# Performance work log

Hardware: AMD Instinct MI355X
Metric: run time of the kernel (lower is better)

The kernel has to match this reference:

```python
import jax, jax.numpy as jnp
import numpy as np

N_NODES = 50000
N_EDGES = 1600000
D_IN, H, Z = 2000, 128, 32
BN_EPS = 1e-5


def setup_inputs() -> dict:
    key = jax.random.key(0)
    ks = jax.random.split(key, 10)
    x = jax.random.normal(ks[0], (N_NODES, D_IN), dtype=jnp.float32)
    edge_index = jax.random.randint(ks[1], (2, N_EDGES), 0, N_NODES, dtype=jnp.int32)
    def xavier(k, shape):
        fan_in, fan_out = shape
        s = jnp.sqrt(6.0 / (fan_in + fan_out))
        return jax.random.uniform(k, shape, jnp.float32, -s, s)
    return {
        "x": x,
        "edge_index": edge_index,
        "W1": xavier(ks[2], (D_IN, H)), "b1": jnp.zeros((H,), jnp.float32),
        "W2": xavier(ks[3], (H, H)),   "b2": jnp.zeros((H,), jnp.float32),
        "g1": jnp.ones((H,), jnp.float32), "be1": jnp.zeros((H,), jnp.float32),
        "g2": jnp.ones((H,), jnp.float32), "be2": jnp.zeros((H,), jnp.float32),
        "Wm": xavier(ks[4], (H, Z)), "bm": jnp.zeros((Z,), jnp.float32),
        "Wv": xavier(ks[5], (H, Z)), "bv": jnp.zeros((Z,), jnp.float32),
        "Wt": xavier(ks[6], (H, 1)), "bt": jnp.zeros((1,), jnp.float32),
        "eps": jax.random.normal(ks[7], (N_NODES, Z), dtype=jnp.float32),
    }


def _gcn_norm(edge_index, n):
    # add self-loops, compute symmetric normalization D^-1/2 A D^-1/2
    loop = jnp.arange(n, dtype=edge_index.dtype)
    src = jnp.concatenate([edge_index[0], loop])
    dst = jnp.concatenate([edge_index[1], loop])
    deg = jax.ops.segment_sum(jnp.ones_like(src, dtype=jnp.float32), dst, num_segments=n)
    dinv = jnp.where(deg > 0, jax.lax.rsqrt(deg), 0.0)
    norm = dinv[src] * dinv[dst]  # [E+N]
    return src, dst, norm


def _gcn(h, W, b, src, dst, norm, n):
    h = h @ W                               # [N, out]
    msg = h[src] * norm[:, None]            # gather + scale, [E+N, out]
    out = jax.ops.segment_sum(msg, dst, num_segments=n)  # scatter-add
    return out + b


def _bn(h, g, b):
    # batch-norm over node dim (training statistics, biased var like torch)
    mu = jnp.mean(h, axis=0)
    var = jnp.mean((h - mu) ** 2, axis=0)
    return g * (h - mu) * jax.lax.rsqrt(var + BN_EPS) + b


def reference(x, edge_index, W1, b1, W2, b2, g1, be1, g2, be2, Wm, bm, Wv, bv, Wt, bt, eps):
    n = x.shape[0]
    src, dst, norm = _gcn_norm(edge_index, n)
    # layer 0: GCN -> BN -> ReLU (dropout = identity in eval)
    h = jax.nn.relu(_bn(_gcn(x, W1, b1, src, dst, norm, n), g1, be1))
    residual = h
    # layer 1
    h = jax.nn.relu(_bn(_gcn(h, W2, b2, src, dst, norm, n), g2, be2))
    h = h + residual
    t = jax.nn.sigmoid(h @ Wt + bt)                       # [N, 1]
    q_m = _gcn(h, Wm, bm, src, dst, norm, n)              # [N, Z]
    q_s = _gcn(h, Wv, bv, src, dst, norm, n)              # [N, Z]
    std = jax.nn.softplus(q_s) + 1e-6
    q_z = q_m + std * eps                                 # Normal(q_m, std).rsample()
    return q_z, q_m, q_s, t
```

## Files before the change

kernel.cpp:

```cpp
#include <hip/hip_runtime.h>
#include <hip/hip_bf16.h>
#include <math.h>

#define N_NODES 50000
#define N_EDGES 1600000
#define DIN     2000
#define HDIM    128
#define ZDIM    32
#define AGG_GRID 782
#define PADROW  50000
#define MAXDEG  96

#define OFF_HA     0UL
#define OFF_HB     12804096UL
#define OFF_H0RES  25608192UL
#define OFF_HMV    38412288UL
#define OFF_W1T    44814336UL
#define OFF_W2T    45338624UL
#define OFF_W3T    45371392UL
#define OFF_CSR    45387776UL
#define OFF_CNT    64587776UL
#define OFF_SUMSA  64787776UL
#define OFF_SUMSB  64788800UL

typedef __attribute__((ext_vector_type(8))) short short8;
typedef __attribute__((ext_vector_type(4))) float f32x4;

__device__ inline unsigned short f2bf(float f) {
    unsigned u = __builtin_bit_cast(unsigned, f);
    u += 0x7FFFu + ((u >> 16) & 1u);
    return (unsigned short)(u >> 16);
}
__device__ inline float bf2f(unsigned short u) {
    return __builtin_bit_cast(float, ((unsigned)u) << 16);
}
__device__ inline void ubf2(unsigned u, float& lo, float& hi) {
    lo = __builtin_bit_cast(float, u << 16);
    hi = __builtin_bit_cast(float, u & 0xFFFF0000u);
}
__device__ inline void unpack8(uint4 v, float* f) {
    ubf2(v.x, f[0], f[1]); ubf2(v.y, f[2], f[3]);
    ubf2(v.z, f[4], f[5]); ubf2(v.w, f[6], f[7]);
}
__device__ inline void gload_lds16(const unsigned short* g, unsigned short* l) {
    __builtin_amdgcn_global_load_lds(
        (const __attribute__((address_space(1))) unsigned int*)g,
        (__attribute__((address_space(3))) unsigned int*)l, 16, 0, 0);
}
__device__ inline f32x4 mfma16(short8 a, short8 b, f32x4 c) {
    return __builtin_amdgcn_mfma_f32_16x16x32_bf16(a, b, c, 0, 0, 0);
}

__global__ void k_prep(const int* __restrict__ e_src, const int* __restrict__ e_dst,
                       const float* __restrict__ W1, const float* __restrict__ W2,
                       const float* __restrict__ Wm, const float* __restrict__ Wv,
                       unsigned short* __restrict__ W1t, unsigned short* __restrict__ W2t,
                       unsigned short* __restrict__ W3t,
                       int* __restrict__ cnt, int* __restrict__ csr,
                       unsigned short* __restrict__ HA, unsigned short* __restrict__ HMV) {
    const int b = blockIdx.x;
    const int tid = threadIdx.x;
    for (int g = b * 256 + tid; g < N_EDGES / 4; g += 1121 * 256) {
        int4 s4 = *(const int4*)(e_src + (size_t)g * 4);
        int4 d4 = *(const int4*)(e_dst + (size_t)g * 4);
        const int ss[4] = {s4.x, s4.y, s4.z, s4.w};
        const int dd[4] = {d4.x, d4.y, d4.z, d4.w};
#pragma unroll
        for (int q = 0; q < 4; ++q) {
            int p = atomicAdd(&cnt[dd[q]], 1);
            if (p < MAXDEG) csr[dd[q] * MAXDEG + p] = ss[q];
        }
    }
    if (b < 1024) {
        int idx = b * 256 + tid;
        int n = idx >> 11, k = idx & 2047;
        W1t[idx] = f2bf((k < DIN) ? W1[(size_t)k * HDIM + n] : 0.f);
    } else if (b < 1088) {
        int idx = (b - 1024) * 256 + tid;
        int n = idx >> 7, k = idx & 127;
        W2t[idx] = f2bf(W2[(size_t)k * HDIM + n]);
    } else if (b < 1120) {
        int idx = (b - 1088) * 256 + tid;
        int n = idx >> 7, k = idx & 127;
        W3t[idx] = f2bf((n < 32) ? Wm[(size_t)k * ZDIM + n]
                                 : Wv[(size_t)k * ZDIM + (n - 32)]);
    } else if (b == 1120) {
        uint4 z = make_uint4(0, 0, 0, 0);
        if (tid < 256)
            *(uint4*)(HA + (size_t)PADROW * HDIM + tid * 8) = z;
        if (tid < 128)
            *(uint4*)(HMV + (size_t)PADROW * 64 + tid * 8) = z;
    }
}

#define G1_BM 64
#define G1_BK 64
__global__ __launch_bounds__(256) void k_gemm1m(const float* __restrict__ A,
        const unsigned short* __restrict__ Bt, const int* __restrict__ cnt,
        unsigned short* __restrict__ C) {
    __shared__ __align__(16) unsigned short Abuf[2][G1_BM * G1_BK];
    __shared__ __align__(16) unsigned short Bbuf[2][HDIM * G1_BK];
    const int tid  = threadIdx.x;
    const int lane = tid & 63;
    const int wave = tid >> 6;
    const int m0   = blockIdx.x * G1_BM;
    const int wm   = (wave >> 1) * 32;
    const int wn   = (wave & 1) * 64;
    const int ar   = tid >> 2;
    const int acp  = tid & 3;

    f32x4 acc[2][4];
#pragma unroll
    for (int i = 0; i < 2; ++i)
#pragma unroll
        for (int j = 0; j < 4; ++j) acc[i][j] = (f32x4)0.f;

    float areg[16];

    auto stageA = [&](int k0) {
        const int g = m0 + ar;
        const int kk = k0 + acp * 16;
        if (g < N_NODES && kk < DIN) {
#pragma unroll
            for (int q = 0; q < 4; ++q)
                *(float4*)&areg[q * 4] = *(const float4*)(A + (size_t)g * DIN + kk + q * 4);
        } else {
#pragma unroll
            for (int q = 0; q < 16; ++q) areg[q] = 0.f;
        }
    };

    auto writeA = [&](int c) {
        unsigned short u[16];
#pragma unroll
        for (int q = 0; q < 16; ++q) u[q] = f2bf(areg[q]);
#pragma unroll
        for (int q = 0; q < 2; ++q) {
            int chunk = acp * 2 + q;
            int pos = chunk ^ (ar & 7);
            *(uint4*)&Abuf[c][ar * G1_BK + pos * 8] = *(const uint4*)&u[q * 8];
        }
    };

    auto issueB = [&](int k0, int c) {
#pragma unroll
        for (int q = 0; q < 4; ++q) {
            int nbase = wave * 32 + q * 8;
            int n = nbase + (lane >> 3);
            int pos = lane & 7;
            int ksrc = k0 + ((pos ^ (n & 7)) * 8);
            gload_lds16(Bt + (size_t)n * 2048 + ksrc, &Bbuf[c][nbase * G1_BK]);
        }
    };

    auto compute = [&](int c) {
        const int rl = lane & 15;
        const int kg = lane >> 4;
#pragma unroll
        for (int ks = 0; ks < 2; ++ks) {
            short8 a[2], b[4];
#pragma unroll
            for (int i = 0; i < 2; ++i) {
                int r = wm + i * 16 + rl;
                int pos = (kg + ks * 4) ^ (r & 7);
                a[i] = *(const short8*)&Abuf[c][r * G1_BK + pos * 8];
            }
#pragma unroll
            for (int j = 0; j < 4; ++j) {
                int n = wn + j * 16 + rl;
                int pos = (kg + ks * 4) ^ (n & 7);
                b[j] = *(const short8*)&Bbuf[c][n * G1_BK + pos * 8];
            }
#pragma unroll
            for (int i = 0; i < 2; ++i)
#pragma unroll
                for (int j = 0; j < 4; ++j)
                    acc[i][j] = mfma16(a[i], b[j], acc[i][j]);
        }
    };

    const int NT = 32;
    stageA(0);
    issueB(0, 0);
#pragma unroll 1
    for (int t = 0; t < NT; ++t) {
        const int c = t & 1;
        writeA(c);
        __syncthreads();
        if (t + 1 < NT) { stageA((t + 1) * G1_BK); issueB((t + 1) * G1_BK, c ^ 1); }
        compute(c);
        __syncthreads();
    }
#pragma unroll
    for (int i = 0; i < 2; ++i) {
        int rb = m0 + wm + i * 16 + (lane >> 4) * 4;
        float dv[4];
#pragma unroll
        for (int r = 0; r < 4; ++r)
            dv[r] = (rb + r < N_NODES) ? rsqrtf((float)(cnt[rb + r] + 1)) : 0.f;
#pragma unroll
        for (int j = 0; j < 4; ++j) {
            int col = wn + j * 16 + (lane & 15);
#pragma unroll
            for (int r = 0; r < 4; ++r)
                if (rb + r < N_NODES)
                    C[(size_t)(rb + r) * HDIM + col] = f2bf(dv[r] * acc[i][j][r]);
        }
    }
}

__global__ __launch_bounds__(256) void k_aggs(const unsigned short* __restrict__ h,
        const int* __restrict__ cnt, const int* __restrict__ csr,
        unsigned short* __restrict__ out, float* __restrict__ sums) {
    __shared__ float redS[8][128];
    __shared__ float redQ[8][128];
    const int tid = threadIdx.x;
    const int slot = tid >> 5;
    const int l32 = tid & 31;
    const int team = l32 >> 4;
    const int lg = l32 & 15;
    const int c = lg * 8;
    float ssum[8] = {}, sq[8] = {};
#pragma unroll 1
    for (int base = blockIdx.x * 8; base < N_NODES; base += AGG_GRID * 8) {
        const int row = base + slot;
        if (row >= N_NODES) continue;
        const int deg = cnt[row];
        const float di = rsqrtf((float)(deg + 1));
        float a[8] = {};
        if (team == 0) {
            float hv[8];
            unpack8(*(const uint4*)(h + (size_t)row * HDIM + c), hv);
#pragma unroll
            for (int i = 0; i < 8; ++i) a[i] = hv[i];
        }
        const int nch = (deg + 3) >> 2;
        const int half = (nch + 1) >> 1;
        const int jb = team ? half : 0;
        const int je = team ? nch : half;
        const int4* csr4 = (const int4*)csr + (size_t)row * (MAXDEG / 4);
        int4 cur = make_int4(PADROW, PADROW, PADROW, PADROW), nxt = cur;
        if (jb < je) cur = csr4[jb];
#pragma unroll 1
        for (int j = jb; j < je; ++j) {
            if (j + 1 < je) nxt = csr4[j + 1];
            const int e0 = 4 * j;
            int s0 = cur.x;
            int s1 = (e0 + 1 < deg) ? cur.y : PADROW;
            int s2 = (e0 + 2 < deg) ? cur.z : PADROW;
            int s3 = (e0 + 3 < deg) ? cur.w : PADROW;
            uint4 g0 = *(const uint4*)(h + (size_t)s0 * HDIM + c);
            uint4 g1 = *(const uint4*)(h + (size_t)s1 * HDIM + c);
            uint4 g2 = *(const uint4*)(h + (size_t)s2 * HDIM + c);
            uint4 g3 = *(const uint4*)(h + (size_t)s3 * HDIM + c);
            float v[8];
            unpack8(g0, v);
#pragma unroll
            for (int i = 0; i < 8; ++i) a[i] += v[i];
            unpack8(g1, v);
#pragma unroll
            for (int i = 0; i < 8; ++i) a[i] += v[i];
            unpack8(g2, v);
#pragma unroll
            for (int i = 0; i < 8; ++i) a[i] += v[i];
            unpack8(g3, v);
#pragma unroll
            for (int i = 0; i < 8; ++i) a[i] += v[i];
            cur = nxt;
        }
#pragma unroll
        for (int i = 0; i < 8; ++i) a[i] += __shfl_xor(a[i], 16);
        if (team == 0) {
            unsigned short o[8];
#pragma unroll
            for (int i = 0; i < 8; ++i) {
                float ov = di * a[i];
                o[i] = f2bf(ov);
                ssum[i] += ov;
                sq[i] += ov * ov;
            }
            *(uint4*)(out + (size_t)row * HDIM + c) = *(const uint4*)o;
        }
    }
    if (team == 0) {
#pragma unroll
        for (int i = 0; i < 8; i += 4) {
            *(float4*)&redS[slot][c + i] = *(const float4*)&ssum[i];
            *(float4*)&redQ[slot][c + i] = *(const float4*)&sq[i];
        }
    }
    __syncthreads();
    if (tid < 128) {
        float s = 0.f, q = 0.f;
#pragma unroll
        for (int g = 0; g < 8; ++g) { s += redS[g][tid]; q += redQ[g][tid]; }
        atomicAdd(&sums[tid], s);
        atomicAdd(&sums[128 + tid], q);
    }
}

__global__ __launch_bounds__(256) void k_gemm2m(const unsigned short* __restrict__ Ain,
        const unsigned short* __restrict__ W2t, const float* __restrict__ sums,
        const float* __restrict__ gg, const float* __restrict__ beta,
        const int* __restrict__ cnt,
        unsigned short* __restrict__ h0res, unsigned short* __restrict__ Hout) {
    __shared__ __align__(16) unsigned short As[64 * 128];
    __shared__ __align__(16) unsigned short Bs[128 * 128];
    __shared__ float prm[256];
    const int tid = threadIdx.x, lane = tid & 63, wave = tid >> 6;
    const int m0 = blockIdx.x * 64;
    if (tid < 128) {
        float mean = sums[tid] * (1.f / N_NODES);
        float var = sums[128 + tid] * (1.f / N_NODES) - mean * mean;
        float rstd = rsqrtf(var + 1e-5f);
        float sc = gg[tid] * rstd;
        prm[tid] = sc;
        prm[128 + tid] = beta[tid] - mean * sc;
    }
    __syncthreads();
    {
        const int ar = tid >> 2, acp = tid & 3;
        const int g = m0 + ar;
        unsigned short u[32];
        if (g < N_NODES) {
#pragma unroll
            for (int q = 0; q < 4; ++q) {
                int kb = acp * 32 + q * 8;
                float v[8];
                unpack8(*(const uint4*)(Ain + (size_t)g * HDIM + kb), v);
#pragma unroll
                for (int e = 0; e < 8; ++e)
                    u[q * 8 + e] = f2bf(fmaxf(v[e] * prm[kb + e] + prm[128 + kb + e], 0.f));
            }
#pragma unroll
            for (int q = 0; q < 4; ++q)
                *(uint4*)(h0res + (size_t)g * HDIM + acp * 32 + q * 8) = *(const uint4*)&u[q * 8];
        } else {
#pragma unroll
            for (int q = 0; q < 32; ++q) u[q] = 0;
        }
#pragma unroll
        for (int q = 0; q < 4; ++q) {
            int ch = acp * 4 + q;
            int pos = ch ^ (ar & 7);
            *(uint4*)&As[ar * 128 + pos * 8] = *(const uint4*)&u[q * 8];
        }
    }
    {
        const int br = tid >> 1, half = tid & 1;
#pragma unroll
        for (int q = 0; q < 8; ++q) {
            int ch = half * 8 + q;
            int pos = ch ^ (br & 7);
            *(uint4*)&Bs[br * 128 + pos * 8] =
                *(const uint4*)(W2t + (size_t)br * 128 + ch * 8);
        }
    }
    __syncthreads();
    const int wm = (wave >> 1) * 32, wn = (wave & 1) * 64;
    const int rl = lane & 15, kg = lane >> 4;
    f32x4 acc[2][4];
#pragma unroll
    for (int i = 0; i < 2; ++i)
#pragma unroll
        for (int j = 0; j < 4; ++j) acc[i][j] = (f32x4)0.f;
#pragma unroll
    for (int ks = 0; ks < 4; ++ks) {
        short8 a[2], b[4];
        int ch = ks * 4 + kg;
#pragma unroll
        for (int i = 0; i < 2; ++i) {
            int r = wm + i * 16 + rl;
            a[i] = *(const short8*)&As[r * 128 + (ch ^ (r & 7)) * 8];
        }
#pragma unroll
        for (int j = 0; j < 4; ++j) {
            int n = wn + j * 16 + rl;
            b[j] = *(const short8*)&Bs[n * 128 + (ch ^ (n & 7)) * 8];
        }
#pragma unroll
        for (int i = 0; i < 2; ++i)
#pragma unroll
            for (int j = 0; j < 4; ++j) acc[i][j] = mfma16(a[i], b[j], acc[i][j]);
    }
#pragma unroll
    for (int i = 0; i < 2; ++i) {
        int rb = m0 + wm + i * 16 + (lane >> 4) * 4;
        float dv[4];
#pragma unroll
        for (int r = 0; r < 4; ++r)
            dv[r] = (rb + r < N_NODES) ? rsqrtf((float)(cnt[rb + r] + 1)) : 0.f;
#pragma unroll
        for (int j = 0; j < 4; ++j) {
            int col = wn + j * 16 + rl;
#pragma unroll
            for (int r = 0; r < 4; ++r)
                if (rb + r < N_NODES)
                    Hout[(size_t)(rb + r) * HDIM + col] = f2bf(dv[r] * acc[i][j][r]);
        }
    }
}

__global__ __launch_bounds__(256) void k_gemm3m(const unsigned short* __restrict__ Ain,
        const unsigned short* __restrict__ h0res, const float* __restrict__ sums,
        const float* __restrict__ gg, const float* __restrict__ beta,
        const unsigned short* __restrict__ W3t, const float* __restrict__ Wt,
        const float* __restrict__ bt, const int* __restrict__ cnt,
        unsigned short* __restrict__ hmv, float* __restrict__ t_out) {
    __shared__ __align__(16) unsigned short As[64 * 128];
    __shared__ __align__(16) unsigned short Bs[64 * 128];
    __shared__ float WtS[128];
    __shared__ float prm[256];
    const int tid = threadIdx.x, lane = tid & 63, wave = tid >> 6;
    const int m0 = blockIdx.x * 64;
    if (tid < 128) {
        float mean = sums[tid] * (1.f / N_NODES);
        float var = sums[128 + tid] * (1.f / N_NODES) - mean * mean;
        float rstd = rsqrtf(var + 1e-5f);
        float sc = gg[tid] * rstd;
        prm[tid] = sc;
        prm[128 + tid] = beta[tid] - mean * sc;
        WtS[tid] = Wt[tid];
    }
    __syncthreads();
    {
        const int ar = tid >> 2, acp = tid & 3;
        const int g = m0 + ar;
        unsigned short u[32];
        if (g < N_NODES) {
#pragma unroll
            for (int q = 0; q < 4; ++q) {
                int kb = acp * 32 + q * 8;
                float v[8], rr[8];
                unpack8(*(const uint4*)(Ain + (size_t)g * HDIM + kb), v);
                unpack8(*(const uint4*)(h0res + (size_t)g * HDIM + kb), rr);
#pragma unroll
                for (int e = 0; e < 8; ++e)
                    u[q * 8 + e] =
                        f2bf(fmaxf(v[e] * prm[kb + e] + prm[128 + kb + e], 0.f) + rr[e]);
            }
        } else {
#pragma unroll
            for (int q = 0; q < 32; ++q) u[q] = 0;
        }
#pragma unroll
        for (int q = 0; q < 4; ++q) {
            int ch = acp * 4 + q;
            int pos = ch ^ (ar & 7);
            *(uint4*)&As[ar * 128 + pos * 8] = *(const uint4*)&u[q * 8];
        }
    }
    {
        const int br = tid >> 2, chq = tid & 3;
#pragma unroll
        for (int q = 0; q < 4; ++q) {
            int ch = chq * 4 + q;
            int pos = ch ^ (br & 7);
            *(uint4*)&Bs[br * 128 + pos * 8] =
                *(const uint4*)(W3t + (size_t)br * 128 + ch * 8);
        }
    }
    __syncthreads();
    const int wm = (wave >> 1) * 32, wn = (wave & 1) * 32;
    const int rl = lane & 15, kg = lane >> 4;
    f32x4 acc[2][2];
#pragma unroll
    for (int i = 0; i < 2; ++i)
#pragma unroll
        for (int j = 0; j < 2; ++j) acc[i][j] = (f32x4)0.f;
#pragma unroll
    for (int ks = 0; ks < 4; ++ks) {
        short8 a[2], b[2];
        int ch = ks * 4 + kg;
#pragma unroll
        for (int i = 0; i < 2; ++i) {
            int r = wm + i * 16 + rl;
            a[i] = *(const short8*)&As[r * 128 + (ch ^ (r & 7)) * 8];
        }
#pragma unroll
        for (int j = 0; j < 2; ++j) {
            int n = wn + j * 16 + rl;
            b[j] = *(const short8*)&Bs[n * 128 + (ch ^ (n & 7)) * 8];
        }
#pragma unroll
        for (int i = 0; i < 2; ++i)
#pragma unroll
            for (int j = 0; j < 2; ++j) acc[i][j] = mfma16(a[i], b[j], acc[i][j]);
    }
#pragma unroll
    for (int i = 0; i < 2; ++i) {
        int rb = m0 + wm + i * 16 + (lane >> 4) * 4;
        float dv[4];
#pragma unroll
        for (int r = 0; r < 4; ++r)
            dv[r] = (rb + r < N_NODES) ? rsqrtf((float)(cnt[rb + r] + 1)) : 0.f;
#pragma unroll
        for (int j = 0; j < 2; ++j) {
            int col = wn + j * 16 + rl;
#pragma unroll
            for (int r = 0; r < 4; ++r)
                if (rb + r < N_NODES)
                    hmv[(size_t)(rb + r) * 64 + col] = f2bf(dv[r] * acc[i][j][r]);
        }
    }
    {
        const int r = wave * 16 + (lane & 15);
        const int sub = lane >> 4;
        float s = 0.f;
#pragma unroll
        for (int q = 0; q < 4; ++q) {
            int ch = sub * 4 + q;
            short8 v = *(const short8*)&As[r * 128 + (ch ^ (r & 7)) * 8];
#pragma unroll
            for (int e = 0; e < 8; ++e)
                s += bf2f((unsigned short)v[e]) * WtS[ch * 8 + e];
        }
        s += __shfl_xor(s, 16);
        s += __shfl_xor(s, 32);
        if (sub == 0 && (m0 + r) < N_NODES)
            t_out[m0 + r] = 1.f / (1.f + expf(-(s + bt[0])));
    }
}

__global__ __launch_bounds__(256) void k_aggfin(const unsigned short* __restrict__ hmv,
        const int* __restrict__ cnt, const int* __restrict__ csr,
        const float* __restrict__ bm, const float* __restrict__ bv,
        const float* __restrict__ eps,
        float* __restrict__ out_qz, float* __restrict__ out_qm,
        float* __restrict__ out_qs) {
    const int tid = threadIdx.x;
    const int slot = tid >> 4;
    const int l16 = tid & 15;
    const int team = l16 >> 3;
    const int l = l16 & 7;
    const int c = l * 8;
#pragma unroll 1
    for (int base = blockIdx.x * 16; base < N_NODES; base += AGG_GRID * 16) {
        const int row = base + slot;
        if (row >= N_NODES) continue;
        const int deg = cnt[row];
        const float di = rsqrtf((float)(deg + 1));
        float a[8] = {};
        if (team == 0) {
            float hv[8];
            unpack8(*(const uint4*)(hmv + (size_t)row * 64 + c), hv);
#pragma unroll
            for (int i = 0; i < 8; ++i) a[i] = hv[i];
        }
        const int nch = (deg + 3) >> 2;
        const int half = (nch + 1) >> 1;
        const int jb = team ? half : 0;
        const int je = team ? nch : half;
        const int4* csr4 = (const int4*)csr + (size_t)row * (MAXDEG / 4);
        int4 cur = make_int4(PADROW, PADROW, PADROW, PADROW), nxt = cur;
        if (jb < je) cur = csr4[jb];
#pragma unroll 1
        for (int j = jb; j < je; ++j) {
            if (j + 1 < je) nxt = csr4[j + 1];
            const int e0 = 4 * j;
            int s0 = cur.x;
            int s1 = (e0 + 1 < deg) ? cur.y : PADROW;
            int s2 = (e0 + 2 < deg) ? cur.z : PADROW;
            int s3 = (e0 + 3 < deg) ? cur.w : PADROW;
            uint4 g0 = *(const uint4*)(hmv + (size_t)s0 * 64 + c);
            uint4 g1 = *(const uint4*)(hmv + (size_t)s1 * 64 + c);
            uint4 g2 = *(const uint4*)(hmv + (size_t)s2 * 64 + c);
            uint4 g3 = *(const uint4*)(hmv + (size_t)s3 * 64 + c);
            float v[8];
            unpack8(g0, v);
#pragma unroll
            for (int i = 0; i < 8; ++i) a[i] += v[i];
            unpack8(g1, v);
#pragma unroll
            for (int i = 0; i < 8; ++i) a[i] += v[i];
            unpack8(g2, v);
#pragma unroll
            for (int i = 0; i < 8; ++i) a[i] += v[i];
            unpack8(g3, v);
#pragma unroll
            for (int i = 0; i < 8; ++i) a[i] += v[i];
            cur = nxt;
        }
#pragma unroll
        for (int i = 0; i < 8; ++i) a[i] += __shfl_xor(a[i], 8);
        const bool lo = l < 4;
        float qv[8];
#pragma unroll
        for (int i = 0; i < 8; ++i)
            qv[i] = di * a[i] + (lo ? bm[c + i] : bv[c - 32 + i]);
        float sp[8] = {};
        if (!lo) {
#pragma unroll
            for (int i = 0; i < 8; ++i)
                sp[i] = fmaxf(qv[i], 0.f) + log1pf(expf(-fabsf(qv[i]))) + 1e-6f;
        }
        float spx[8];
#pragma unroll
        for (int i = 0; i < 8; ++i) spx[i] = __shfl_xor(sp[i], 4);
        if (team == 0) {
            if (lo) {
                *(float4*)(out_qm + (size_t)row * 32 + c) = *(const float4*)&qv[0];
                *(float4*)(out_qm + (size_t)row * 32 + c + 4) = *(const float4*)&qv[4];
                float e[8];
                *(float4*)&e[0] = *(const float4*)(eps + (size_t)row * 32 + c);
                *(float4*)&e[4] = *(const float4*)(eps + (size_t)row * 32 + c + 4);
                float qz[8];
#pragma unroll
                for (int i = 0; i < 8; ++i) qz[i] = qv[i] + spx[i] * e[i];
                *(float4*)(out_qz + (size_t)row * 32 + c) = *(const float4*)&qz[0];
                *(float4*)(out_qz + (size_t)row * 32 + c + 4) = *(const float4*)&qz[4];
            } else {
                *(float4*)(out_qs + (size_t)row * 32 + (c - 32)) = *(const float4*)&qv[0];
                *(float4*)(out_qs + (size_t)row * 32 + (c - 32) + 4) = *(const float4*)&qv[4];
            }
        }
    }
}

extern "C" void kernel_launch(void* const* d_in, const int* in_sizes, int n_in,
                              void* d_out, int out_size, void* d_ws, size_t ws_size,
                              hipStream_t stream) {
    (void)in_sizes; (void)n_in; (void)out_size; (void)ws_size;
    const float* x   = (const float*)d_in[0];
    const int*   ei  = (const int*)d_in[1];
    const float* W1  = (const float*)d_in[2];
    const float* W2  = (const float*)d_in[4];
    const float* g1  = (const float*)d_in[6];
    const float* be1 = (const float*)d_in[7];
    const float* g2  = (const float*)d_in[8];
    const float* be2 = (const float*)d_in[9];
    const float* Wm  = (const float*)d_in[10];
    const float* bm  = (const float*)d_in[11];
    const float* Wv  = (const float*)d_in[12];
    const float* bv  = (const float*)d_in[13];
    const float* Wt  = (const float*)d_in[14];
    const float* bt  = (const float*)d_in[15];
    const float* eps = (const float*)d_in[16];

    const int* e_src = ei;
    const int* e_dst = ei + N_EDGES;

    char* ws = (char*)d_ws;
    unsigned short* HA    = (unsigned short*)(ws + OFF_HA);
    unsigned short* HB    = (unsigned short*)(ws + OFF_HB);
    unsigned short* H0RES = (unsigned short*)(ws + OFF_H0RES);
    unsigned short* HMV   = (unsigned short*)(ws + OFF_HMV);
    unsigned short* W1t   = (unsigned short*)(ws + OFF_W1T);
    unsigned short* W2t   = (unsigned short*)(ws + OFF_W2T);
    unsigned short* W3t   = (unsigned short*)(ws + OFF_W3T);
    int*   csr     = (int*)(ws + OFF_CSR);
    int*   cnt     = (int*)(ws + OFF_CNT);
    float* sumsA   = (float*)(ws + OFF_SUMSA);
    float* sumsB   = (float*)(ws + OFF_SUMSB);

    float* out_qz = (float*)d_out;
    float* out_qm = out_qz + N_NODES * ZDIM;
    float* out_qs = out_qm + N_NODES * ZDIM;
    float* out_t  = out_qs + N_NODES * ZDIM;

    const int MB = (N_NODES + 63) / 64;

    hipMemsetAsync(ws + OFF_CNT, 0, 200000, stream);
    hipMemsetAsync(ws + OFF_SUMSA, 0, 2048, stream);
    k_prep<<<1121, 256, 0, stream>>>(e_src, e_dst, W1, W2, Wm, Wv,
                                     W1t, W2t, W3t, cnt, csr, HA, HMV);
    k_gemm1m<<<MB, 256, 0, stream>>>(x, W1t, cnt, HA);
    k_aggs<<<AGG_GRID, 256, 0, stream>>>(HA, cnt, csr, HB, sumsA);
    k_gemm2m<<<MB, 256, 0, stream>>>(HB, W2t, sumsA, g1, be1, cnt, H0RES, HA);
    k_aggs<<<AGG_GRID, 256, 0, stream>>>(HA, cnt, csr, HB, sumsB);
    k_gemm3m<<<MB, 256, 0, stream>>>(HB, H0RES, sumsB, g2, be2, W3t, Wt, bt,
                                     cnt, HMV, out_t);
    k_aggfin<<<AGG_GRID, 256, 0, stream>>>(HMV, cnt, csr, bm, bv, eps,
                                           out_qz, out_qm, out_qs);
}
```

Measured before the change: 463.7 us.

## Partition aggregation columns by XCD and deepen GEMM1 A-prefetch to two tiles

The aggregation kernel now gives each block a 32-column quarter of the feature dimension. Block indices are mapped so that each group of XCDs (block id mod 8) always handles the same column quarter, which shrinks the per-XCD L2 working set for the gathered neighbor rows. It also regroups threads so that 8 threads cover one row, 32 rows per block, and reduces the BN statistics per quarter. Separately, GEMM1 keeps two register buffers for A and prefetches two k-tiles ahead to hide global load latency, at the cost of more registers and extra loop unrolling.

Result: slower. 475.5 us (+2.6%).

```diff
diff --git a/kernel.cpp b/kernel.cpp
--- a/kernel.cpp
+++ b/kernel.cpp
@@ -8,6 +8,7 @@
 #define HDIM    128
 #define ZDIM    32
 #define AGG_GRID 782
+#define AGQ_GRID 1024
 #define PADROW  50000
 #define MAXDEG  96
 
@@ -115,25 +116,25 @@
 #pragma unroll
         for (int j = 0; j < 4; ++j) acc[i][j] = (f32x4)0.f;
 
-    float areg[16];
-
-    auto stageA = [&](int k0) {
+    float areg0[16], areg1[16];
+
+    auto stageA = [&](int k0, float* a) {
         const int g = m0 + ar;
         const int kk = k0 + acp * 16;
         if (g < N_NODES && kk < DIN) {
 #pragma unroll
             for (int q = 0; q < 4; ++q)
-                *(float4*)&areg[q * 4] = *(const float4*)(A + (size_t)g * DIN + kk + q * 4);
+                *(float4*)&a[q * 4] = *(const float4*)(A + (size_t)g * DIN + kk + q * 4);
         } else {
 #pragma unroll
-            for (int q = 0; q < 16; ++q) areg[q] = 0.f;
+            for (int q = 0; q < 16; ++q) a[q] = 0.f;
         }
     };
 
-    auto writeA = [&](int c) {
+    auto writeA = [&](int c, const float* a) {
         unsigned short u[16];
 #pragma unroll
-        for (int q = 0; q < 16; ++q) u[q] = f2bf(areg[q]);
+        for (int q = 0; q < 16; ++q) u[q] = f2bf(a[q]);
 #pragma unroll
         for (int q = 0; q < 2; ++q) {
             int chunk = acp * 2 + q;
@@ -180,15 +181,22 @@
     };
 
     const int NT = 32;
-    stageA(0);
+    stageA(0, areg0);
+    stageA(G1_BK, areg1);
     issueB(0, 0);
 #pragma unroll 1
-    for (int t = 0; t < NT; ++t) {
-        const int c = t & 1;
-        writeA(c);
+    for (int tt = 0; tt < NT; tt += 2) {
+        writeA(0, areg0);
         __syncthreads();
-        if (t + 1 < NT) { stageA((t + 1) * G1_BK); issueB((t + 1) * G1_BK, c ^ 1); }
-        compute(c);
+        if (tt + 1 < NT) issueB((tt + 1) * G1_BK, 1);
+        if (tt + 2 < NT) stageA((tt + 2) * G1_BK, areg0);
+        compute(0);
+        __syncthreads();
+        writeA(1, areg1);
+        __syncthreads();
+        if (tt + 2 < NT) issueB((tt + 2) * G1_BK, 0);
+        if (tt + 3 < NT) stageA((tt + 3) * G1_BK, areg1);
+        compute(1);
         __syncthreads();
     }
 #pragma unroll
@@ -212,17 +220,21 @@
 __global__ __launch_bounds__(256) void k_aggs(const unsigned short* __restrict__ h,
         const int* __restrict__ cnt, const int* __restrict__ csr,
         unsigned short* __restrict__ out, float* __restrict__ sums) {
-    __shared__ float redS[8][128];
-    __shared__ float redQ[8][128];
+    __shared__ float redS[32][32];
+    __shared__ float redQ[32][32];
     const int tid = threadIdx.x;
-    const int slot = tid >> 5;
-    const int l32 = tid & 31;
-    const int team = l32 >> 4;
-    const int lg = l32 & 15;
-    const int c = lg * 8;
+    const int slot = tid >> 3;
+    const int l8 = tid & 7;
+    const int team = l8 >> 2;
+    const int l4 = l8 & 3;
+    const int b = blockIdx.x;
+    const int xcd = b & 7;
+    const int q = xcd & 3;
+    const int c = q * 32 + l4 * 8;
+    const int rgrp = (b >> 3) * 2 + (xcd >> 2);
     float ssum[8] = {}, sq[8] = {};
 #pragma unroll 1
-    for (int base = blockIdx.x * 8; base < N_NODES; base += AGG_GRID * 8) {
+    for (int base = rgrp * 32; base < N_NODES; base += 256 * 32) {
         const int row = base + slot;
         if (row >= N_NODES) continue;
         const int deg = cnt[row];
@@ -269,7 +281,7 @@
             cur = nxt;
         }
 #pragma unroll
-        for (int i = 0; i < 8; ++i) a[i] += __shfl_xor(a[i], 16);
+        for (int i = 0; i < 8; ++i) a[i] += __shfl_xor(a[i], 4);
         if (team == 0) {
             unsigned short o[8];
 #pragma unroll
@@ -285,17 +297,17 @@
     if (team == 0) {
 #pragma unroll
         for (int i = 0; i < 8; i += 4) {
-            *(float4*)&redS[slot][c + i] = *(const float4*)&ssum[i];
-            *(float4*)&redQ[slot][c + i] = *(const float4*)&sq[i];
+            *(float4*)&redS[slot][l4 * 8 + i] = *(const float4*)&ssum[i];
+            *(float4*)&redQ[slot][l4 * 8 + i] = *(const float4*)&sq[i];
         }
     }
     __syncthreads();
-    if (tid < 128) {
-        float s = 0.f, q = 0.f;
-#pragma unroll
-        for (int g = 0; g < 8; ++g) { s += redS[g][tid]; q += redQ[g][tid]; }
-        atomicAdd(&sums[tid], s);
-        atomicAdd(&sums[128 + tid], q);
+    if (tid < 32) {
+        float s = 0.f, qq = 0.f;
+#pragma unroll
+        for (int g = 0; g < 32; ++g) { s += redS[g][tid]; qq += redQ[g][tid]; }
+        atomicAdd(&sums[q * 32 + tid], s);
+        atomicAdd(&sums[128 + q * 32 + tid], qq);
     }
 }
 
@@ -665,9 +677,9 @@
     k_prep<<<1121, 256, 0, stream>>>(e_src, e_dst, W1, W2, Wm, Wv,
                                      W1t, W2t, W3t, cnt, csr, HA, HMV);
     k_gemm1m<<<MB, 256, 0, stream>>>(x, W1t, cnt, HA);
-    k_aggs<<<AGG_GRID, 256, 0, stream>>>(HA, cnt, csr, HB, sumsA);
+    k_aggs<<<AGQ_GRID, 256, 0, stream>>>(HA, cnt, csr, HB, sumsA);
     k_gemm2m<<<MB, 256, 0, stream>>>(HB, W2t, sumsA, g1, be1, cnt, H0RES, HA);
-    k_aggs<<<AGG_GRID, 256, 0, stream>>>(HA, cnt, csr, HB, sumsB);
+    k_aggs<<<AGQ_GRID, 256, 0, stream>>>(HA, cnt, csr, HB, sumsB);
     k_gemm3m<<<MB, 256, 0, stream>>>(HB, H0RES, sumsB, g2, be2, W3t, Wt, bt,
                                      cnt, HMV, out_t);
     k_aggfin<<<AGG_GRID, 256, 0, stream>>>(HMV, cnt, csr, bm, bv, eps,
```
